# Optimization experiments

Measured on AMD Instinct MI355X. Metric: run time of the kernel, lower is better.

Reference implementation:

```python
import jax, jax.numpy as jnp
import numpy as np

B, T, H, NH, EL = 64, 1024, 256, 4, 768
DH = H // NH
EPS = 1e-3


def _ln(x, g, b):
    mu = jnp.mean(x, axis=-1, keepdims=True)
    var = jnp.var(x, axis=-1, keepdims=True)
    return (x - mu) * jax.lax.rsqrt(var + EPS) * g + b


def _glu(x, W, b):
    y = x @ W.T + b
    a, gate = jnp.split(y, 2, axis=-1)
    return a * jax.nn.sigmoid(gate)


def setup_inputs() -> dict:
    key = jax.random.key(0)
    ks = iter(jax.random.split(key, 40))
    w = lambda *s: jax.random.normal(next(ks), s, jnp.float32) * 0.02
    inp = {
        "temporal_features": jax.random.normal(next(ks), (B, T, H), jnp.float32),
        "ce": jax.random.normal(next(ks), (B, H), jnp.float32),
        # enrichment GRN (with context)
        "eg_Wa": w(H, H), "eg_ba": jnp.zeros((H,), jnp.float32),
        "eg_Wc": w(H, H),
        "eg_Wi": w(H, H), "eg_bi": jnp.zeros((H,), jnp.float32),
        "eg_Wg": w(2 * H, H), "eg_bg": jnp.zeros((2 * H,), jnp.float32),
        "eg_lng": jnp.ones((H,), jnp.float32), "eg_lnb": jnp.zeros((H,), jnp.float32),
        # interpretable MHA
        "att_Wqkv": w((2 * NH + 1) * DH, H),
        "att_Wout": w(H, DH),
        # attention gate + LN
        "ag_W": w(2 * H, H), "ag_b": jnp.zeros((2 * H,), jnp.float32),
        "aln_g": jnp.ones((H,), jnp.float32), "aln_b": jnp.zeros((H,), jnp.float32),
        # positionwise GRN (no context)
        "pg_Wa": w(H, H), "pg_ba": jnp.zeros((H,), jnp.float32),
        "pg_Wi": w(H, H), "pg_bi": jnp.zeros((H,), jnp.float32),
        "pg_Wg": w(2 * H, H), "pg_bg": jnp.zeros((2 * H,), jnp.float32),
        "pg_lng": jnp.ones((H,), jnp.float32), "pg_lnb": jnp.zeros((H,), jnp.float32),
        # decoder gate + LN
        "dg_W": w(2 * H, H), "dg_b": jnp.zeros((2 * H,), jnp.float32),
        "dln_g": jnp.ones((H,), jnp.float32), "dln_b": jnp.zeros((H,), jnp.float32),
    }
    return inp


def _forward(temporal_features, ce,
             eg_Wa, eg_ba, eg_Wc, eg_Wi, eg_bi, eg_Wg, eg_bg, eg_lng, eg_lnb,
             att_Wqkv, att_Wout,
             ag_W, ag_b, aln_g, aln_b,
             pg_Wa, pg_ba, pg_Wi, pg_bi, pg_Wg, pg_bg, pg_lng, pg_lnb,
             dg_W, dg_b, dln_g, dln_b):
    # enrichment GRN: linear + context -> ELU -> linear -> GLU -> residual -> LN
    x = temporal_features @ eg_Wa.T + eg_ba + (ce @ eg_Wc.T)[:, None, :]
    x = jax.nn.elu(x)
    x = x @ eg_Wi.T + eg_bi
    x = _glu(x, eg_Wg, eg_bg)
    enriched = _ln(x + temporal_features, eg_lng, eg_lnb)

    # interpretable multi-head attention (shared V, head-averaged output)
    qkv = enriched @ att_Wqkv.T  # [B,T,(2*NH+1)*DH]
    q = qkv[..., : NH * DH].reshape(B, T, NH, DH)
    k = qkv[..., NH * DH: 2 * NH * DH].reshape(B, T, NH, DH)
    v = qkv[..., 2 * NH * DH:]  # [B,T,DH]
    scale = DH ** -0.5
    scores = jnp.einsum("bthd,bshd->bhts", q, k) * scale  # [B,NH,T,T]
    mask = jnp.triu(jnp.full((T, T), -jnp.inf, jnp.float32), k=1)
    probs = jax.nn.softmax(scores + mask, axis=-1)
    attn_vec = jnp.einsum("bhts,bsd->bhtd", probs, v)  # [B,NH,T,DH]
    m_attn = jnp.mean(attn_vec, axis=1)  # [B,T,DH]
    a = m_attn @ att_Wout.T  # [B,T,H]

    # slice to decoder steps
    a = a[:, EL:, :]
    tf_dec = temporal_features[:, EL:, :]
    enr_dec = enriched[:, EL:, :]

    x = _glu(a, ag_W, ag_b)
    x = _ln(x + enr_dec, aln_g, aln_b)

    # positionwise GRN
    y = jax.nn.elu(x @ pg_Wa.T + pg_ba)
    y = y @ pg_Wi.T + pg_bi
    y = _glu(y, pg_Wg, pg_bg)
    x = _ln(y + x, pg_lng, pg_lnb)

    x = _glu(x, dg_W, dg_b)
    x = _ln(x + tf_dec, dln_g, dln_b)
    return x


def reference(temporal_features, ce,
              eg_Wa, eg_ba, eg_Wc, eg_Wi, eg_bi, eg_Wg, eg_bg, eg_lng, eg_lnb,
              att_Wqkv, att_Wout,
              ag_W, ag_b, aln_g, aln_b,
              pg_Wa, pg_ba, pg_Wi, pg_bi, pg_Wg, pg_bg, pg_lng, pg_lnb,
              dg_W, dg_b, dln_g, dln_b):
    return _forward(temporal_features, ce,
                    eg_Wa, eg_ba, eg_Wc, eg_Wi, eg_bi, eg_Wg, eg_bg, eg_lng, eg_lnb,
                    att_Wqkv, att_Wout,
                    ag_W, ag_b, aln_g, aln_b,
                    pg_Wa, pg_ba, pg_Wi, pg_bi, pg_Wg, pg_bg, pg_lng, pg_lnb,
                    dg_W, dg_b, dln_g, dln_b)
```

## Files before the change

kernel.cpp:

```cpp
#include <hip/hip_runtime.h>
#include <hip/hip_bf16.h>
#include <math.h>

typedef __hip_bfloat16 bf16;
typedef unsigned short u16;
typedef unsigned int u32;
typedef __attribute__((ext_vector_type(8))) short bfrag8;
typedef __attribute__((ext_vector_type(8))) _Float16 hfrag8;
typedef __attribute__((ext_vector_type(4))) float f32x4;

constexpr int Bb = 64, Tt = 1024, Hh = 256, NHn = 4, DHd = 64, ELe = 768;
constexpr int TD = Tt - ELe;
constexpr int BT = Bb * Tt;
constexpr int BD = Bb * TD;
constexpr float QSCALE = 0.18033688011112042f;

__device__ __forceinline__ bool probe_bf16(const void* probe) {
    return *(const unsigned int*)probe == 0x3F803F80u;
}
__device__ __forceinline__ float bfbits2f(unsigned short u) {
    union { unsigned int i; float f; } c; c.i = ((unsigned int)u) << 16; return c.f;
}
__device__ __forceinline__ u16 f2bf(float f) {
    union { float f; unsigned int u; } c; c.f = f;
    unsigned int r = c.u + 0x7fffu + ((c.u >> 16) & 1u);
    return (u16)(r >> 16);
}
__device__ __forceinline__ u16 f2h(float f) {
    union { _Float16 h; u16 u; } c; c.h = (_Float16)f; return c.u;
}
__device__ __forceinline__ float h2f(u16 u) {
    union { u16 u; _Float16 h; } c; c.u = u; return (float)c.h;
}
__device__ __forceinline__ float4 load4dt(const void* p, long idx, bool bf) {
    if (bf) {
        ushort4 u = *(const ushort4*)((const unsigned short*)p + idx);
        return make_float4(bfbits2f(u.x), bfbits2f(u.y), bfbits2f(u.z), bfbits2f(u.w));
    }
    return *(const float4*)((const float*)p + idx);
}
__device__ __forceinline__ float load1dt(const void* p, long idx, bool bf) {
    return bf ? bfbits2f(((const unsigned short*)p)[idx]) : ((const float*)p)[idx];
}
__device__ __forceinline__ int swz(int row, int k) {
    return row * 64 + ((((k >> 3) ^ (row & 7)) << 3) | (k & 7));
}
__device__ __forceinline__ void gload16(const void* g, void* l) {
    __builtin_amdgcn_global_load_lds(
        (const __attribute__((address_space(1))) void*)g,
        (__attribute__((address_space(3))) void*)l, 16, 0, 0);
}
__device__ __forceinline__ u32 cvtpk(float a, float b) {
    u32 r; asm("v_cvt_pk_bf16_f32 %0, %1, %2" : "=v"(r) : "v"(a), "v"(b)); return r;
}

__global__ __launch_bounds__(256) void cvt_f16(const void* __restrict__ src,
                                               u16* __restrict__ dst,
                                               long n4, const void* __restrict__ probe)
{
    const bool dtb = probe_bf16(probe);
    long i = (long)blockIdx.x * 256 + threadIdx.x;
    long stride = (long)gridDim.x * 256;
    for (; i < n4; i += stride) {
        float4 v = load4dt(src, i * 4, dtb);
        ushort4 o = make_ushort4(f2h(v.x), f2h(v.y), f2h(v.z), f2h(v.w));
        *(ushort4*)&dst[i * 4] = o;
    }
}

__global__ __launch_bounds__(256) void cvtw_all(
    const void* s0, const void* s1, const void* s2, const void* s3,
    const void* s4, const void* s5, const void* s6, const void* s7,
    const void* s8, const void* s9, u16* __restrict__ dst,
    const void* __restrict__ probe)
{
    const bool dtb = probe_bf16(probe);
    int blk = blockIdx.x;
    const void* src; long seg0, base;
    if      (blk < 64)  { src = s0; seg0 = 0;   base = 0;      }
    else if (blk < 128) { src = s1; seg0 = 64;  base = 65536;  }
    else if (blk < 256) { src = s2; seg0 = 128; base = 131072; }
    else if (blk < 400) { src = s3; seg0 = 256; base = 262144; }
    else if (blk < 416) { src = s4; seg0 = 400; base = 409600; }
    else if (blk < 544) { src = s5; seg0 = 416; base = 425984; }
    else if (blk < 608) { src = s6; seg0 = 544; base = 557056; }
    else if (blk < 672) { src = s7; seg0 = 608; base = 622592; }
    else if (blk < 800) { src = s8; seg0 = 672; base = 688128; }
    else                { src = s9; seg0 = 800; base = 819200; }
    long i = (long)(blk - seg0) * 1024 + (long)threadIdx.x * 4;
    float4 v = load4dt(src, i, dtb);
    ushort4 o = make_ushort4(f2h(v.x), f2h(v.y), f2h(v.z), f2h(v.w));
    *(ushort4*)&dst[base + i] = o;
}

__global__ __launch_bounds__(256) void ceproj_kernel(const void* __restrict__ ce,
                                                     const void* __restrict__ Wc,
                                                     const void* __restrict__ probe,
                                                     float* __restrict__ out)
{
    const bool bf = probe_bf16(probe);
    __shared__ float ces[256];
    int b = blockIdx.x, tid = threadIdx.x;
    ces[tid] = load1dt(ce, b * 256 + tid, bf);
    __syncthreads();
    float acc = 0.f;
    #pragma unroll 4
    for (int k = 0; k < 256; k += 4) {
        float4 w4 = load4dt(Wc, (long)tid * 256 + k, bf);
        acc = fmaf(ces[k], w4.x, acc);
        acc = fmaf(ces[k + 1], w4.y, acc);
        acc = fmaf(ces[k + 2], w4.z, acc);
        acc = fmaf(ces[k + 3], w4.w, acc);
    }
    out[b * 256 + tid] = acc;
}


__global__ __launch_bounds__(256, 3) void gemm_mfma(
    const u16* __restrict__ A_g, const u16* __restrict__ W_g,
    const void* __restrict__ bias,
    const float* __restrict__ ceproj,
    const void* __restrict__ res0,
    void* __restrict__ Cout,
    const void* __restrict__ probe,
    int M, int N, int K, int mode,
    int res_kind, int a_decmap, int res_decmap, int out_kind)
{
    const bool dtb = probe_bf16(probe);
    const int tid = threadIdx.x;
    const int w = tid >> 6, lane = tid & 63, lr = lane & 15, lg = lane >> 4;
    const int wm = w >> 1, wn = w & 1;
    const int m0 = blockIdx.x * 128;
    const int n0 = blockIdx.y * 128;
    const int n0g = blockIdx.y * 64;

    __shared__ __align__(16) u16 AsF[128 * 64];
    __shared__ __align__(16) u16 WsF[128 * 64];

    const int sl8 = lane >> 3;
    const int slot = lane & 7;

    long aoff[4]; long woff[4];
    #pragma unroll
    for (int i = 0; i < 4; ++i) {
        int row = w * 32 + i * 8 + sl8;
        int gm = m0 + row;
        long ar = a_decmap ? ((long)(gm >> 8) * 1024 + 768 + (gm & 255)) : (long)gm;
        aoff[i] = ar * K + (long)((slot ^ (row & 7)) * 8);
        int wr;
        if (mode == 3) {
            int g = row >> 5;
            wr = ((g & 1) ? 256 : 0) + n0g + ((g >> 1) << 5) + (row & 31);
        } else {
            wr = n0 + row; if (wr > N - 1) wr = N - 1;
        }
        woff[i] = (long)wr * K + (long)((slot ^ (row & 7)) * 8);
    }

    f32x4 acc[4][4];
    #pragma unroll
    for (int i = 0; i < 4; ++i)
        #pragma unroll
        for (int j = 0; j < 4; ++j) acc[i][j] = (f32x4){0.f, 0.f, 0.f, 0.f};

    for (int kt = 0; kt < K; kt += 64) {
        __syncthreads();
        #pragma unroll
        for (int i = 0; i < 4; ++i) {
            int rbase = w * 32 + i * 8;
            gload16(A_g + aoff[i] + kt, &AsF[rbase * 64]);
            gload16(W_g + woff[i] + kt, &WsF[rbase * 64]);
        }
        __syncthreads();

        #pragma unroll
        for (int kh = 0; kh < 2; ++kh) {
            hfrag8 wf[4];
            #pragma unroll
            for (int j = 0; j < 4; ++j)
                wf[j] = *(const hfrag8*)&WsF[swz(wn * 64 + j * 16 + lr, kh * 32 + lg * 8)];
            #pragma unroll
            for (int i = 0; i < 4; ++i) {
                hfrag8 ah = *(const hfrag8*)&AsF[swz(wm * 64 + i * 16 + lr, kh * 32 + lg * 8)];
                #pragma unroll
                for (int j = 0; j < 4; ++j)
                    acc[i][j] = __builtin_amdgcn_mfma_f32_16x16x32_f16(ah, wf[j], acc[i][j], 0, 0, 0);
            }
        }
    }

    #pragma unroll
    for (int i = 0; i < 4; ++i) {
        #pragma unroll
        for (int r = 0; r < 4; ++r) {
            int gm = m0 + wm * 64 + i * 16 + lg * 4 + r;
            if (mode == 3) {
                long rrow = res_decmap ? ((long)(gm >> 8) * 1024 + 768 + (gm & 255)) : (long)gm;
                #pragma unroll
                for (int jj = 0; jj < 2; ++jj) {
                    int c = n0g + wn * 32 + jj * 16 + lr;
                    float a = acc[i][jj][r]     + load1dt(bias, c, dtb);
                    float g = acc[i][jj + 2][r] + load1dt(bias, c + 256, dtb);
                    float rv;
                    if (res_kind == 1) rv = h2f(((const u16*)res0)[rrow * 256 + c]);
                    else               rv = load1dt(res0, rrow * 256 + c, dtb);
                    float o = a / (1.f + __expf(-g)) + rv;
                    long ci = (long)gm * 256 + c;
                    if (out_kind == 2) ((u16*)Cout)[ci] = f2h(o);
                    else               ((float*)Cout)[ci] = o;
                }
            } else {
                #pragma unroll
                for (int j = 0; j < 4; ++j) {
                    int n = n0 + wn * 64 + j * 16 + lr;
                    if (n < N) {
                        float v = acc[i][j][r];
                        if (bias) v += load1dt(bias, n, dtb);
                        if (mode == 1) v += ceproj[((gm >> 10) << 8) + n];
                        if (mode >= 1) v = (v > 0.f) ? v : (__expf(v) - 1.f);
                        long ci = (long)gm * N + n;
                        if (out_kind == 0)      ((float*)Cout)[ci] = v;
                        else if (out_kind == 1) ((u16*)Cout)[ci] = f2bf(v);
                        else if (out_kind == 3) ((u16*)Cout)[ci] = f2bf(v * QSCALE);
                        else                    ((u16*)Cout)[ci] = f2h(v);
                    }
                }
            }
        }
    }
}

__global__ __launch_bounds__(256, 4) void gemm_mfma64(
    const u16* __restrict__ A_g, const u16* __restrict__ W_g,
    const void* __restrict__ bias,
    const float* __restrict__ ceproj,
    const void* __restrict__ res0,
    void* __restrict__ Cout,
    const void* __restrict__ probe,
    int M, int N, int K, int mode,
    int res_kind, int a_decmap, int res_decmap, int out_kind)
{
    const bool dtb = probe_bf16(probe);
    const int tid = threadIdx.x;
    const int w = tid >> 6, lane = tid & 63, lr = lane & 15, lg = lane >> 4;
    const int wm = w >> 1, wn = w & 1;
    const int m0 = blockIdx.x * 64;
    const int n0 = blockIdx.y * 128;
    const int n0g = blockIdx.y * 64;

    __shared__ __align__(16) u16 AsF[64 * 64];
    __shared__ __align__(16) u16 WsF[128 * 64];

    const int sl8 = lane >> 3, slot = lane & 7;

    long aoff[2]; long woff[4];
    #pragma unroll
    for (int i = 0; i < 2; ++i) {
        int row = i * 32 + w * 8 + sl8;
        int gm = m0 + row;
        long ar = a_decmap ? ((long)(gm >> 8) * 1024 + 768 + (gm & 255)) : (long)gm;
        aoff[i] = ar * K + (long)((slot ^ (row & 7)) * 8);
    }
    #pragma unroll
    for (int i = 0; i < 4; ++i) {
        int row = i * 32 + w * 8 + sl8;
        int wr;
        if (mode == 3) {
            int g = row >> 5;
            wr = ((g & 1) ? 256 : 0) + n0g + ((g >> 1) << 5) + (row & 31);
        } else {
            wr = n0 + row; if (wr > N - 1) wr = N - 1;
        }
        woff[i] = (long)wr * K + (long)((slot ^ (row & 7)) * 8);
    }

    f32x4 acc[2][4];
    #pragma unroll
    for (int i = 0; i < 2; ++i)
        #pragma unroll
        for (int j = 0; j < 4; ++j) acc[i][j] = (f32x4){0.f, 0.f, 0.f, 0.f};

    for (int kt = 0; kt < K; kt += 64) {
        __syncthreads();
        #pragma unroll
        for (int i = 0; i < 2; ++i)
            gload16(A_g + aoff[i] + kt, &AsF[(i * 32 + w * 8) * 64]);
        #pragma unroll
        for (int i = 0; i < 4; ++i)
            gload16(W_g + woff[i] + kt, &WsF[(i * 32 + w * 8) * 64]);
        __syncthreads();

        #pragma unroll
        for (int kh = 0; kh < 2; ++kh) {
            hfrag8 wf[4];
            #pragma unroll
            for (int j = 0; j < 4; ++j)
                wf[j] = *(const hfrag8*)&WsF[swz(wn * 64 + j * 16 + lr, kh * 32 + lg * 8)];
            #pragma unroll
            for (int i = 0; i < 2; ++i) {
                hfrag8 ah = *(const hfrag8*)&AsF[swz(wm * 32 + i * 16 + lr, kh * 32 + lg * 8)];
                #pragma unroll
                for (int j = 0; j < 4; ++j)
                    acc[i][j] = __builtin_amdgcn_mfma_f32_16x16x32_f16(ah, wf[j], acc[i][j], 0, 0, 0);
            }
        }
    }

    #pragma unroll
    for (int i = 0; i < 2; ++i) {
        #pragma unroll
        for (int r = 0; r < 4; ++r) {
            int gm = m0 + wm * 32 + i * 16 + lg * 4 + r;
            if (mode == 3) {
                long rrow = res_decmap ? ((long)(gm >> 8) * 1024 + 768 + (gm & 255)) : (long)gm;
                #pragma unroll
                for (int jj = 0; jj < 2; ++jj) {
                    int c = n0g + wn * 32 + jj * 16 + lr;
                    float a = acc[i][jj][r]     + load1dt(bias, c, dtb);
                    float g = acc[i][jj + 2][r] + load1dt(bias, c + 256, dtb);
                    float rv;
                    if (res_kind == 1) rv = h2f(((const u16*)res0)[rrow * 256 + c]);
                    else               rv = load1dt(res0, rrow * 256 + c, dtb);
                    float o = a / (1.f + __expf(-g)) + rv;
                    long ci = (long)gm * 256 + c;
                    if (out_kind == 2) ((u16*)Cout)[ci] = f2h(o);
                    else               ((float*)Cout)[ci] = o;
                }
            } else {
                #pragma unroll
                for (int j = 0; j < 4; ++j) {
                    int n = n0 + wn * 64 + j * 16 + lr;
                    if (n < N) {
                        float v = acc[i][j][r];
                        if (bias) v += load1dt(bias, n, dtb);
                        if (mode == 1) v += ceproj[((gm >> 10) << 8) + n];
                        if (mode >= 1) v = (v > 0.f) ? v : (__expf(v) - 1.f);
                        long ci = (long)gm * N + n;
                        if (out_kind == 0)      ((float*)Cout)[ci] = v;
                        else if (out_kind == 1) ((u16*)Cout)[ci] = f2bf(v);
                        else if (out_kind == 3) ((u16*)Cout)[ci] = f2bf(v * QSCALE);
                        else                    ((u16*)Cout)[ci] = f2h(v);
                    }
                }
            }
        }
    }
}

__global__ __launch_bounds__(256) void ln_kernel(const u16* __restrict__ vin,
                                                 const void* __restrict__ g,
                                                 const void* __restrict__ beta,
                                                 void* __restrict__ out,
                                                 const void* __restrict__ probe,
                                                 int out_kind)
{
    const bool dtb = probe_bf16(probe);
    int tid = threadIdx.x;
    long m = (long)blockIdx.x * 4 + (tid >> 6);
    int l = tid & 63;
    ushort4 raw = *(const ushort4*)&vin[m * 256 + l * 4];
    float v0 = h2f(raw.x), v1 = h2f(raw.y), v2 = h2f(raw.z), v3 = h2f(raw.w);
    float s  = v0 + v1 + v2 + v3;
    float s2 = v0 * v0 + v1 * v1 + v2 * v2 + v3 * v3;
    #pragma unroll
    for (int off = 32; off > 0; off >>= 1) {
        s  += __shfl_xor(s, off);
        s2 += __shfl_xor(s2, off);
    }
    float mu  = s * (1.f / 256.f);
    float var = s2 * (1.f / 256.f) - mu * mu;
    float rstd = rsqrtf(var + 1e-3f);
    float4 gg = load4dt(g, l * 4, dtb);
    float4 bb = load4dt(beta, l * 4, dtb);
    float y0 = (v0 - mu) * rstd * gg.x + bb.x;
    float y1 = (v1 - mu) * rstd * gg.y + bb.y;
    float y2 = (v2 - mu) * rstd * gg.z + bb.z;
    float y3 = (v3 - mu) * rstd * gg.w + bb.w;
    long idx = m * 256 + l * 4;
    if (out_kind == 2) {
        *(ushort4*)&((u16*)out)[idx] = make_ushort4(f2h(y0), f2h(y1), f2h(y2), f2h(y3));
    } else if (dtb) {
        *(ushort4*)&((u16*)out)[idx] = make_ushort4(f2bf(y0), f2bf(y1), f2bf(y2), f2bf(y3));
    } else {
        *(float4*)&((float*)out)[idx] = make_float4(y0, y1, y2, y3);
    }
}

__global__ __launch_bounds__(256) void vtrans(const u16* __restrict__ vtmp,
                                              u16* __restrict__ vt)
{
    int b  = blockIdx.x >> 4;
    int s0 = (blockIdx.x & 15) << 6;
    __shared__ u16 t[64][72];
    int tid = threadIdx.x;
    {
        int sl = tid >> 4;
        int d0 = (tid & 15) << 2;
        #pragma unroll
        for (int u = 0; u < 4; ++u) {
            int s = u * 16 + sl;
            ushort4 v4 = *(const ushort4*)&vtmp[((long)(b * 1024 + s0 + s)) * 64 + d0];
            t[d0 + 0][s] = v4.x; t[d0 + 1][s] = v4.y;
            t[d0 + 2][s] = v4.z; t[d0 + 3][s] = v4.w;
        }
    }
    __syncthreads();
    {
        int d = tid >> 2, c0 = (tid & 3) << 4;
        u16* dst = vt + ((long)(b * 64 + d)) * 1024 + s0 + c0;
        *(uint4*)dst       = *(const uint4*)&t[d][c0];
        *(uint4*)(dst + 8) = *(const uint4*)&t[d][c0 + 8];
    }
}

__global__ __launch_bounds__(256) void attn_mfma(const u16* __restrict__ qd,
                                                 const u16* __restrict__ kb,
                                                 const u16* __restrict__ vt,
                                                 float* __restrict__ Oscr)
{
    int bid = blockIdx.x;
    int qt = bid & 3, h = (bid >> 2) & 3, b = bid >> 4;
    int tid = threadIdx.x;
    int w = tid >> 6, lane = tid & 63, lr = lane & 15, lg = lane >> 4;
    const int sl8 = lane >> 3, slot = lane & 7;

    __shared__ __align__(16) u16 Ks[2][64 * 64];
    __shared__ __align__(16) u16 Vs[2][64 * 64];

    bfrag8 qf0, qf1;
    {
        long tok = (long)b * 256 + qt * 64 + w * 16 + lr;
        const u16* qp = qd + tok * 256 + h * 64 + lg * 8;
        qf0 = *(const bfrag8*)(qp);
        qf1 = *(const bfrag8*)(qp + 32);
    }

    f32x4 O[4];
    float m_i = -INFINITY, l_i = 0.f;
    #pragma unroll
    for (int jd = 0; jd < 4; ++jd) O[jd] = (f32x4){0.f, 0.f, 0.f, 0.f};
    const int qabs = 768 + qt * 64 + w * 16 + lr;

    const int srcA = lr + ((lg & 1) ? 32 : 0);
    const int srcB = srcA + 16;
    const bool hi = (lg >= 2);
    const int ntiles = 13 + qt;

    const long kbase = (long)b * 1024 * 256 + h * 64;
    const long vbase = (long)b * 64 * 1024;

    #pragma unroll
    for (int i = 0; i < 2; ++i) {
        int rbase = w * 16 + i * 8;
        int row = rbase + sl8;
        int sw = (slot ^ (row & 7)) * 8;
        gload16(kb + kbase + (long)row * 256 + sw, &Ks[0][rbase * 64]);
        gload16(vt + vbase + (long)row * 1024 + sw, &Vs[0][rbase * 64]);
    }

    int cur = 0;
    for (int st = 0; st < ntiles; ++st) {
        int s0 = st * 64;
        __syncthreads();
        if (st + 1 < ntiles) {
            int s1 = s0 + 64;
            #pragma unroll
            for (int i = 0; i < 2; ++i) {
                int rbase = w * 16 + i * 8;
                int row = rbase + sl8;
                int sw = (slot ^ (row & 7)) * 8;
                gload16(kb + kbase + (long)(s1 + row) * 256 + sw, &Ks[cur ^ 1][rbase * 64]);
                gload16(vt + vbase + (long)row * 1024 + s1 + sw, &Vs[cur ^ 1][rbase * 64]);
            }
        }

        f32x4 sv[4];
        #pragma unroll
        for (int jb = 0; jb < 4; ++jb) {
            f32x4 a = (f32x4){0.f, 0.f, 0.f, 0.f};
            a = __builtin_amdgcn_mfma_f32_16x16x32_bf16(
                    *(const bfrag8*)&Ks[cur][swz(jb * 16 + lr, lg * 8)], qf0, a, 0, 0, 0);
            a = __builtin_amdgcn_mfma_f32_16x16x32_bf16(
                    *(const bfrag8*)&Ks[cur][swz(jb * 16 + lr, 32 + lg * 8)], qf1, a, 0, 0, 0);
            sv[jb] = a;
        }

        if (st == ntiles - 1) {
            #pragma unroll
            for (int jb = 0; jb < 4; ++jb)
                #pragma unroll
                for (int r = 0; r < 4; ++r)
                    if (s0 + jb * 16 + lg * 4 + r > qabs) sv[jb][r] = -INFINITY;
        }

        float mx = -INFINITY;
        #pragma unroll
        for (int jb = 0; jb < 4; ++jb)
            #pragma unroll
            for (int r = 0; r < 4; ++r) mx = fmaxf(mx, sv[jb][r]);
        mx = fmaxf(mx, __shfl_xor(mx, 16));
        mx = fmaxf(mx, __shfl_xor(mx, 32));
        float mnew = fmaxf(m_i, mx);
        float alpha = exp2f(m_i - mnew);
        float ps = 0.f;
        #pragma unroll
        for (int jb = 0; jb < 4; ++jb)
            #pragma unroll
            for (int r = 0; r < 4; ++r) {
                float p = exp2f(sv[jb][r] - mnew);
                sv[jb][r] = p; ps += p;
            }
        ps += __shfl_xor(ps, 16);
        ps += __shfl_xor(ps, 32);
        l_i = l_i * alpha + ps;
        m_i = mnew;

        float alr[4];
        #pragma unroll
        for (int r = 0; r < 4; ++r) alr[r] = __shfl(alpha, lg * 4 + r);
        #pragma unroll
        for (int jd = 0; jd < 4; ++jd)
            #pragma unroll
            for (int r = 0; r < 4; ++r) O[jd][r] *= alr[r];

        u32 c0_[2], c1_[2], c2_[2], c3_[2];
        c0_[0] = cvtpk(sv[0][0], sv[0][1]); c0_[1] = cvtpk(sv[0][2], sv[0][3]);
        c1_[0] = cvtpk(sv[1][0], sv[1][1]); c1_[1] = cvtpk(sv[1][2], sv[1][3]);
        c2_[0] = cvtpk(sv[2][0], sv[2][1]); c2_[1] = cvtpk(sv[2][2], sv[2][3]);
        c3_[0] = cvtpk(sv[3][0], sv[3][1]); c3_[1] = cvtpk(sv[3][2], sv[3][3]);

        #pragma unroll
        for (int sh = 0; sh < 2; ++sh) {
            u32 lo0 = sh ? c2_[0] : c0_[0], lo1 = sh ? c2_[1] : c0_[1];
            u32 hi0 = sh ? c3_[0] : c1_[0], hi1 = sh ? c3_[1] : c1_[1];
            u32 a0 = (u32)__shfl((int)lo0, srcA), a1 = (u32)__shfl((int)lo1, srcA);
            u32 A0 = (u32)__shfl((int)hi0, srcA), A1 = (u32)__shfl((int)hi1, srcA);
            u32 b0 = (u32)__shfl((int)lo0, srcB), b1 = (u32)__shfl((int)lo1, srcB);
            u32 B0 = (u32)__shfl((int)hi0, srcB), B1 = (u32)__shfl((int)hi1, srcB);
            union { u32 u[4]; bfrag8 v; } pu;
            pu.u[0] = hi ? A0 : a0; pu.u[1] = hi ? A1 : a1;
            pu.u[2] = hi ? B0 : b0; pu.u[3] = hi ? B1 : b1;
            #pragma unroll
            for (int jd = 0; jd < 4; ++jd) {
                bfrag8 vb = *(const bfrag8*)&Vs[cur][swz(jd * 16 + lr, sh * 32 + lg * 8)];
                O[jd] = __builtin_amdgcn_mfma_f32_16x16x32_bf16(pu.v, vb, O[jd], 0, 0, 0);
            }
        }
        cur ^= 1;
    }

    float inv = 1.f / l_i;
    float linv[4];
    #pragma unroll
    for (int r = 0; r < 4; ++r) linv[r] = __shfl(inv, lg * 4 + r);
    #pragma unroll
    for (int jd = 0; jd < 4; ++jd)
        #pragma unroll
        for (int r = 0; r < 4; ++r) {
            long token = (long)b * 256 + qt * 64 + w * 16 + lg * 4 + r;
            Oscr[token * 256 + h * 64 + jd * 16 + lr] = O[jd][r] * linv[r];
        }
}

__global__ __launch_bounds__(256) void headmean(const float* __restrict__ O,
                                                u16* __restrict__ outH)
{
    int i = blockIdx.x * 256 + threadIdx.x;
    int token = i >> 6, d = i & 63;
    const float* p = O + (long)token * 256 + d;
    float m = 0.25f * (p[0] + p[64] + p[128] + p[192]);
    outH[i] = f2h(m);
}

extern "C" void kernel_launch(void* const* d_in, const int* in_sizes, int n_in,
                              void* d_out, int out_size, void* d_ws, size_t ws_size,
                              hipStream_t stream)
{
    const void* tf       = d_in[0];
    const void* ce       = d_in[1];
    const void* eg_Wa    = d_in[2];
    const void* eg_ba    = d_in[3];
    const void* eg_Wc    = d_in[4];
    const void* eg_Wi    = d_in[5];
    const void* eg_bi    = d_in[6];
    const void* eg_Wg    = d_in[7];
    const void* eg_bg    = d_in[8];
    const void* eg_lng   = d_in[9];
    const void* eg_lnb   = d_in[10];
    const void* att_Wqkv = d_in[11];
    const void* att_Wout = d_in[12];
    const void* ag_W     = d_in[13];
    const void* ag_b     = d_in[14];
    const void* aln_g    = d_in[15];
    const void* aln_b    = d_in[16];
    const void* pg_Wa    = d_in[17];
    const void* pg_ba    = d_in[18];
    const void* pg_Wi    = d_in[19];
    const void* pg_bi    = d_in[20];
    const void* pg_Wg    = d_in[21];
    const void* pg_bg    = d_in[22];
    const void* pg_lng   = d_in[23];
    const void* pg_lnb   = d_in[24];
    const void* dg_W     = d_in[25];
    const void* dg_b     = d_in[26];
    const void* dln_g    = d_in[27];
    const void* dln_b    = d_in[28];
    const void* probe    = eg_lng;

    float* ws = (float*)d_ws;

    const long CEP = 0;
    const long WPo = 65536;
    const long P   = 1114112;
    const long Q   = P + 8388608L;
    const long T   = Q + 16777216L;

    float* ceprojF = ws + CEP;

    u16* wp = (u16*)(ws + WPo);
    u16* WaH = wp + 0;      u16* WiH = wp + 65536;  u16* WgH = wp + 131072;
    u16* WqH = wp + 262144; u16* WoH = wp + 409600; u16* AgH = wp + 425984;
    u16* PaH = wp + 557056; u16* PiH = wp + 622592; u16* PgH = wp + 688128;
    u16* DgH = wp + 819200;

    u16* tfH   = (u16*)(ws + T);
    u16* g1H   = (u16*)(ws + Q);
    u16* x2H   = (u16*)(ws + Q + 8388608L);
    u16* glu3H = (u16*)(ws + Q);
    u16* enrH  = (u16*)(ws + T);

    u16*   kvbK = (u16*)(ws + Q);
    u16*   vtmp = (u16*)(ws + Q + 8388608L);
    u16*   qd16 = (u16*)(ws + Q + 10485760L);
    u16*   vt16 = (u16*)(ws + Q + 12582912L);
    float* Oscr = ws + P;
    u16*   matnH = (u16*)(ws + P + 4194304L);

    u16* D[8];
    for (int k = 0; k < 8; ++k) D[k] = (u16*)(ws + Q + (long)k * 2097152L);

    dim3 blk(256);
    auto cgrid = [](long n4) {
        long g = (n4 + 255) / 256; if (g > 2048) g = 2048; return dim3((unsigned)g);
    };
    const long NBT = (long)BT * 256;

    cvt_f16<<<cgrid(NBT / 4), blk, 0, stream>>>(tf, tfH, NBT / 4, probe);
    cvtw_all<<<928, blk, 0, stream>>>(eg_Wa, eg_Wi, eg_Wg, att_Wqkv, att_Wout,
                                      ag_W, pg_Wa, pg_Wi, pg_Wg, dg_W, wp, probe);
    ceproj_kernel<<<64, blk, 0, stream>>>(ce, eg_Wc, probe, ceprojF);

    gemm_mfma<<<dim3(BT / 128, 2), blk, 0, stream>>>(
        tfH, WaH, eg_ba, ceprojF, nullptr, g1H, probe, BT, 256, 256, 1, 0, 0, 0, 2);
    gemm_mfma<<<dim3(BT / 128, 2), blk, 0, stream>>>(
        g1H, WiH, eg_bi, nullptr, nullptr, x2H, probe, BT, 256, 256, 0, 0, 0, 0, 2);
    gemm_mfma<<<dim3(BT / 128, 4), blk, 0, stream>>>(
        x2H, WgH, eg_bg, nullptr, tf, glu3H, probe, BT, 256, 256, 3, 0, 0, 0, 2);
    ln_kernel<<<BT / 4, blk, 0, stream>>>(glu3H, eg_lng, eg_lnb, enrH, probe, 2);

    gemm_mfma<<<dim3(BT / 128, 2), blk, 0, stream>>>(
        enrH, WqH + (long)256 * 256, nullptr, nullptr, nullptr, kvbK, probe,
        BT, 256, 256, 0, 0, 0, 0, 1);
    gemm_mfma<<<dim3(BT / 128, 1), blk, 0, stream>>>(
        enrH, WqH + (long)512 * 256, nullptr, nullptr, nullptr, vtmp, probe,
        BT, 64, 256, 0, 0, 0, 0, 1);
    gemm_mfma64<<<dim3(BD / 64, 2), blk, 0, stream>>>(
        enrH, WqH, nullptr, nullptr, nullptr, qd16, probe,
        BD, 256, 256, 0, 0, 1, 0, 3);
    vtrans<<<1024, blk, 0, stream>>>(vtmp, vt16);

    attn_mfma<<<Bb * NHn * 4, blk, 0, stream>>>(qd16, kvbK, vt16, Oscr);
    headmean<<<(BD * 64) / 256, blk, 0, stream>>>(Oscr, matnH);

    gemm_mfma64<<<dim3(BD / 64, 2), blk, 0, stream>>>(
        matnH, WoH, nullptr, nullptr, nullptr, D[0], probe, BD, 256, 64, 0, 0, 0, 0, 2);
    gemm_mfma64<<<dim3(BD / 64, 4), blk, 0, stream>>>(
        D[0], AgH, ag_b, nullptr, enrH, D[1], probe, BD, 256, 256, 3, 1, 0, 1, 2);
    ln_kernel<<<BD / 4, blk, 0, stream>>>(D[1], aln_g, aln_b, D[2], probe, 2);
    gemm_mfma64<<<dim3(BD / 64, 2), blk, 0, stream>>>(
        D[2], PaH, pg_ba, nullptr, nullptr, D[3], probe, BD, 256, 256, 2, 0, 0, 0, 2);
    gemm_mfma64<<<dim3(BD / 64, 2), blk, 0, stream>>>(
        D[3], PiH, pg_bi, nullptr, nullptr, D[4], probe, BD, 256, 256, 0, 0, 0, 0, 2);
    gemm_mfma64<<<dim3(BD / 64, 4), blk, 0, stream>>>(
        D[4], PgH, pg_bg, nullptr, D[2], D[5], probe, BD, 256, 256, 3, 1, 0, 0, 2);
    ln_kernel<<<BD / 4, blk, 0, stream>>>(D[5], pg_lng, pg_lnb, D[6], probe, 2);
    gemm_mfma64<<<dim3(BD / 64, 4), blk, 0, stream>>>(
        D[6], DgH, dg_b, nullptr, tf, D[7], probe, BD, 256, 256, 3, 0, 0, 1, 2);
    ln_kernel<<<BD / 4, blk, 0, stream>>>(D[7], dln_g, dln_b, d_out, probe, 1);
}
```

Baseline: 553.6 us.

## Double-buffer GEMM LDS tiles with K-step 32 to overlap loads and MFMA

The MFMA GEMM now splits its shared-memory A/W tiles into two buffers of K=32 each, in place of one K=64 tile, and uses a matching XOR swizzle. The next K-slice is issued via global_load_lds while the current slice feeds the MFMAs, leaving one barrier per iteration. This aims to hide global-load latency behind compute. The cost is twice as many loop iterations and barriers, and correctness relies on the barrier waiting for the async LDS loads to finish.

```diff
diff --git a/kernel.cpp b/kernel.cpp
--- a/kernel.cpp
+++ b/kernel.cpp
@@ -44,6 +44,9 @@
 }
 __device__ __forceinline__ int swz(int row, int k) {
     return row * 64 + ((((k >> 3) ^ (row & 7)) << 3) | (k & 7));
+}
+__device__ __forceinline__ int swz32(int row, int k) {
+    return row * 32 + ((((k >> 3) ^ ((row >> 1) & 3)) << 3) | (k & 7));
 }
 __device__ __forceinline__ void gload16(const void* g, void* l) {
     __builtin_amdgcn_global_load_lds(
@@ -115,7 +118,6 @@
     out[b * 256 + tid] = acc;
 }
 
-
 __global__ __launch_bounds__(256, 3) void gemm_mfma(
     const u16* __restrict__ A_g, const u16* __restrict__ W_g,
     const void* __restrict__ bias,
@@ -134,19 +136,19 @@
     const int n0 = blockIdx.y * 128;
     const int n0g = blockIdx.y * 64;
 
-    __shared__ __align__(16) u16 AsF[128 * 64];
-    __shared__ __align__(16) u16 WsF[128 * 64];
-
-    const int sl8 = lane >> 3;
-    const int slot = lane & 7;
-
-    long aoff[4]; long woff[4];
-    #pragma unroll
-    for (int i = 0; i < 4; ++i) {
-        int row = w * 32 + i * 8 + sl8;
+    __shared__ __align__(16) u16 AsF[2][128 * 32];
+    __shared__ __align__(16) u16 WsF[2][128 * 32];
+
+    const int srow16 = lane >> 2;
+    const int slot = lane & 3;
+
+    long aoff[2]; long woff[2];
+    #pragma unroll
+    for (int i = 0; i < 2; ++i) {
+        int row = w * 32 + i * 16 + srow16;
         int gm = m0 + row;
         long ar = a_decmap ? ((long)(gm >> 8) * 1024 + 768 + (gm & 255)) : (long)gm;
-        aoff[i] = ar * K + (long)((slot ^ (row & 7)) * 8);
+        aoff[i] = ar * K + (long)((slot ^ ((row >> 1) & 3)) * 8);
         int wr;
         if (mode == 3) {
             int g = row >> 5;
@@ -154,7 +156,7 @@
         } else {
             wr = n0 + row; if (wr > N - 1) wr = N - 1;
         }
-        woff[i] = (long)wr * K + (long)((slot ^ (row & 7)) * 8);
+        woff[i] = (long)wr * K + (long)((slot ^ ((row >> 1) & 3)) * 8);
     }
 
     f32x4 acc[4][4];
@@ -163,30 +165,36 @@
         #pragma unroll
         for (int j = 0; j < 4; ++j) acc[i][j] = (f32x4){0.f, 0.f, 0.f, 0.f};
 
-    for (int kt = 0; kt < K; kt += 64) {
+    #pragma unroll
+    for (int i = 0; i < 2; ++i) {
+        int rbase = w * 32 + i * 16;
+        gload16(A_g + aoff[i], &AsF[0][rbase * 32]);
+        gload16(W_g + woff[i], &WsF[0][rbase * 32]);
+    }
+
+    int cur = 0;
+    for (int kt = 0; kt < K; kt += 32) {
         __syncthreads();
+        if (kt + 32 < K) {
+            #pragma unroll
+            for (int i = 0; i < 2; ++i) {
+                int rbase = w * 32 + i * 16;
+                gload16(A_g + aoff[i] + kt + 32, &AsF[cur ^ 1][rbase * 32]);
+                gload16(W_g + woff[i] + kt + 32, &WsF[cur ^ 1][rbase * 32]);
+            }
+        }
+        hfrag8 wf[4];
+        #pragma unroll
+        for (int j = 0; j < 4; ++j)
+            wf[j] = *(const hfrag8*)&WsF[cur][swz32(wn * 64 + j * 16 + lr, lg * 8)];
         #pragma unroll
         for (int i = 0; i < 4; ++i) {
-            int rbase = w * 32 + i * 8;
-            gload16(A_g + aoff[i] + kt, &AsF[rbase * 64]);
-            gload16(W_g + woff[i] + kt, &WsF[rbase * 64]);
-        }
-        __syncthreads();
-
-        #pragma unroll
-        for (int kh = 0; kh < 2; ++kh) {
-            hfrag8 wf[4];
+            hfrag8 ah = *(const hfrag8*)&AsF[cur][swz32(wm * 64 + i * 16 + lr, lg * 8)];
             #pragma unroll
             for (int j = 0; j < 4; ++j)
-                wf[j] = *(const hfrag8*)&WsF[swz(wn * 64 + j * 16 + lr, kh * 32 + lg * 8)];
-            #pragma unroll
-            for (int i = 0; i < 4; ++i) {
-                hfrag8 ah = *(const hfrag8*)&AsF[swz(wm * 64 + i * 16 + lr, kh * 32 + lg * 8)];
-                #pragma unroll
-                for (int j = 0; j < 4; ++j)
-                    acc[i][j] = __builtin_amdgcn_mfma_f32_16x16x32_f16(ah, wf[j], acc[i][j], 0, 0, 0);
-            }
-        }
+                acc[i][j] = __builtin_amdgcn_mfma_f32_16x16x32_f16(ah, wf[j], acc[i][j], 0, 0, 0);
+        }
+        cur ^= 1;
     }
 
     #pragma unroll
```

After: 545.9 us. No clear change (-1.4%).
